# Kernel optimization log

Measured on AMD Instinct MI355X. Metric: run time of the kernel, lower is better.

Reference implementation:

```python
import jax, jax.numpy as jnp
import numpy as np

N = 100000
NEG_SLOPE = 0.2
EPS = 1e-16


def _gatconv(h_in, src, dst, W, a_src, a_dst, b):
    # h_in: [N, Fin]; src/dst: [E_tot] (self-loops included); W: [Fin, Fout]
    h = h_in @ W                                  # [N, Fout]
    alpha_s = h @ a_src                           # [N]
    alpha_d = h @ a_dst                           # [N]
    e = alpha_s[src] + alpha_d[dst]               # [E_tot]
    e = jnp.where(e > 0, e, NEG_SLOPE * e)        # leaky_relu
    m = jax.ops.segment_max(e, dst, num_segments=N)
    e = jnp.exp(e - m[dst])
    s = jax.ops.segment_sum(e, dst, num_segments=N)
    alpha = e / (s[dst] + EPS)                    # segment softmax over in-edges of each dst
    out = jax.ops.segment_sum(alpha[:, None] * h[src], dst, num_segments=N)
    return out + b


def setup_inputs() -> dict:
    key = jax.random.key(0)
    ks = jax.random.split(key, 10)
    Fin, Fh, Fo = 64, 64, 40
    E = 1600000
    x = jax.random.normal(ks[0], (N, Fin), dtype=jnp.float32)
    edge_index = jax.random.randint(ks[1], (2, E), 0, N, dtype=jnp.int64)
    g = 1.0 / np.sqrt(Fin)
    W1 = jax.random.uniform(ks[2], (Fin, Fh), jnp.float32, -g, g)
    a_src1 = jax.random.uniform(ks[3], (Fh,), jnp.float32, -g, g)
    a_dst1 = jax.random.uniform(ks[4], (Fh,), jnp.float32, -g, g)
    b1 = jnp.zeros((Fh,), jnp.float32)
    g2 = 1.0 / np.sqrt(Fh)
    W2 = jax.random.uniform(ks[5], (Fh, Fo), jnp.float32, -g2, g2)
    a_src2 = jax.random.uniform(ks[6], (Fo,), jnp.float32, -g2, g2)
    a_dst2 = jax.random.uniform(ks[7], (Fo,), jnp.float32, -g2, g2)
    b2 = jnp.zeros((Fo,), jnp.float32)
    return {"x": x, "edge_index": edge_index, "W1": W1, "a_src1": a_src1,
            "a_dst1": a_dst1, "b1": b1, "W2": W2, "a_src2": a_src2,
            "a_dst2": a_dst2, "b2": b2}


def reference(x, edge_index, W1, a_src1, a_dst1, b1, W2, a_src2, a_dst2, b2):
    # add self loops (PyG GATConv default)
    loops = jnp.arange(N, dtype=edge_index.dtype)
    src = jnp.concatenate([edge_index[0], loops])
    dst = jnp.concatenate([edge_index[1], loops])
    h = _gatconv(x, src, dst, W1, a_src1, a_dst1, b1)
    h = jax.nn.relu(h)  # dropout p=0 / eval -> no-op
    h = _gatconv(h, src, dst, W2, a_src2, a_dst2, b2)
    return jax.nn.log_softmax(h, axis=-1)
```

## Files before the change

### kernel.cpp

```cpp
#include <hip/hip_runtime.h>
#include <math.h>

#ifndef NEG_SLOPE
#define NEG_SLOPE 0.2f
#endif

#define BUCK_BITS 9
#define BUCK_SIZE 512
#define BUCK_CAP  12288
#define PA_ILP    8

__device__ __forceinline__ void get_edge(const void* ei, int is64, int e, int E,
                                         int& s, int& d) {
    if (e >= E) { s = e - E; d = s; return; }
    if (is64) {
        const long long* p = (const long long*)ei;
        s = (int)p[e];
        d = (int)p[(long long)E + e];
    } else {
        const int* p = (const int*)ei;
        s = p[e];
        d = p[E + e];
    }
}

__device__ __forceinline__ unsigned f2bf1(float x) {
    unsigned u = __float_as_uint(x);
    return (u + 0x7fffu + ((u >> 16) & 1u)) >> 16;
}

__global__ __launch_bounds__(256) void bin_gemm1(
    const void* __restrict__ ei, int E, int Etot, int binB,
    int* __restrict__ fill, int2* __restrict__ pairs,
    const float* __restrict__ x, const float* __restrict__ W1,
    const float* __restrict__ avs, const float* __restrict__ avd,
    unsigned short* __restrict__ Hb, float* __restrict__ asn,
    float* __restrict__ adn, int N) {
    __shared__ __align__(16) char smem[34816];
    const int t = threadIdx.x;

    if ((int)blockIdx.x < binB) {
        int* cnt   = (int*)smem;
        int* goff  = cnt + 256;
        int* sflag = goff + 256;
        if (t < 64) {
            const int* p = (const int*)ei;
            int bad = 0;
            for (int j = 0; j < 4; ++j) bad |= (p[2 * (t * 4 + j) + 1] != 0);
            unsigned long long m = __ballot(bad);
            if (t == 0) *sflag = (m == 0ull) ? 1 : 0;
        }
        cnt[t] = 0;
        __syncthreads();
        const int is64 = *sflag;
        const int base = blockIdx.x * (256 * PA_ILP) + t;
        int s[PA_ILP], d[PA_ILP], r[PA_ILP];
        bool ok[PA_ILP];
#pragma unroll
        for (int u = 0; u < PA_ILP; ++u) {
            int e = base + u * 256;
            ok[u] = (e < Etot);
            s[u] = d[u] = 0;
            if (ok[u]) get_edge(ei, is64, e, E, s[u], d[u]);
        }
#pragma unroll
        for (int u = 0; u < PA_ILP; ++u)
            if (ok[u]) r[u] = atomicAdd(&cnt[d[u] >> BUCK_BITS], 1);
        __syncthreads();
        if (cnt[t] > 0) goff[t] = atomicAdd(&fill[t], cnt[t]);
        __syncthreads();
#pragma unroll
        for (int u = 0; u < PA_ILP; ++u) {
            if (ok[u]) {
                int b = d[u] >> BUCK_BITS;
                int idx = goff[b] + r[u];
                if (idx < BUCK_CAP)
                    pairs[(size_t)b * BUCK_CAP + idx] = make_int2(s[u], d[u]);
            }
        }
    } else {
        constexpr int K = 64, F = 64, TPR = 4, R = 64, C = 16;
        float* sW  = (float*)smem;
        float* sA  = sW + K * F;
        float* sas = sA + R * (K + 4);
        float* sad = sas + F;

        for (int i = t; i < K * F / 4; i += 256)
            ((float4*)sW)[i] = ((const float4*)W1)[i];
        for (int i = t; i < F; i += 256) { sas[i] = avs[i]; sad[i] = avd[i]; }

        const int base = (blockIdx.x - binB) * R;
        for (int i = t; i < R * (K / 4); i += 256) {
            int row = i >> 4;
            int c4  = i & 15;
            float4 v = make_float4(0.f, 0.f, 0.f, 0.f);
            if (base + row < N)
                v = ((const float4*)(x + (size_t)(base + row) * K))[c4];
            float* dp = &sA[row * (K + 4) + c4 * 4];
            dp[0] = v.x; dp[1] = v.y; dp[2] = v.z; dp[3] = v.w;
        }
        __syncthreads();

        const int r  = t / TPR;
        const int f0 = (t % TPR) * C;
        float acc[C];
#pragma unroll
        for (int j = 0; j < C; ++j) acc[j] = 0.f;
        const float* sa = &sA[r * (K + 4)];
#pragma unroll
        for (int k = 0; k < K; ++k) {
            float av = sa[k];
            const float* w = &sW[k * F + f0];
#pragma unroll
            for (int j = 0; j < C; ++j) acc[j] += av * w[j];
        }
        float ps = 0.f, pd = 0.f;
#pragma unroll
        for (int j = 0; j < C; ++j) { ps += acc[j] * sas[f0 + j]; pd += acc[j] * sad[f0 + j]; }
#pragma unroll
        for (int off = 1; off < TPR; off <<= 1) {
            ps += __shfl_xor(ps, off);
            pd += __shfl_xor(pd, off);
        }
        const int row = base + r;
        if (row < N) {
            if ((t % TPR) == 0) { asn[row] = ps; adn[row] = pd; }
            unsigned* hp = (unsigned*)(Hb + (size_t)row * F + f0);
#pragma unroll
            for (int j = 0; j < C / 2; ++j)
                hp[j] = f2bf1(acc[2 * j]) | (f2bf1(acc[2 * j + 1]) << 16);
        }
    }
}

__global__ __launch_bounds__(256) void bucket_csr(
    const int2* __restrict__ pairs, const int* __restrict__ fill,
    int* __restrict__ row_ptr, int* __restrict__ csr_src, int N, int nbuck) {
    __shared__ int cnt[BUCK_SIZE];
    __shared__ int offs[BUCK_SIZE];
    __shared__ int sbase[256];
    __shared__ int stot;
    const int t = threadIdx.x;
    if (t < 64) {
        int v[4];
        int loc = 0;
#pragma unroll
        for (int i = 0; i < 4; ++i) {
            int idx = t * 4 + i;
            v[i] = (idx < nbuck) ? fill[idx] : 0;
            loc += v[i];
        }
        int x = loc;
        for (int off = 1; off < 64; off <<= 1) {
            int y = __shfl_up(x, off);
            if (t >= off) x += y;
        }
        int run = x - loc;
#pragma unroll
        for (int i = 0; i < 4; ++i) {
            int idx = t * 4 + i;
            if (idx < 256) sbase[idx] = run;
            run += v[i];
        }
        if (t == 63) stot = x;
    }
    cnt[t] = 0; cnt[t + 256] = 0;
    __syncthreads();

    const int b = blockIdx.x;
    const int base_d = b << BUCK_BITS;
    const int gb = sbase[b];
    int m = fill[b];
    if (m > BUCK_CAP) m = BUCK_CAP;
    if (b == 0 && t == 0) row_ptr[N] = stot;
    const int2* bp = pairs + (size_t)b * BUCK_CAP;

    int i = t;
    for (; i + 768 < m; i += 1024) {
        int2 p0 = bp[i], p1 = bp[i + 256], p2 = bp[i + 512], p3 = bp[i + 768];
        atomicAdd(&cnt[p0.y - base_d], 1);
        atomicAdd(&cnt[p1.y - base_d], 1);
        atomicAdd(&cnt[p2.y - base_d], 1);
        atomicAdd(&cnt[p3.y - base_d], 1);
    }
    for (; i < m; i += 256) atomicAdd(&cnt[bp[i].y - base_d], 1);
    __syncthreads();

    if (t < 64) {
        int v[8];
        int loc = 0;
#pragma unroll
        for (int j = 0; j < 8; ++j) { v[j] = cnt[t * 8 + j]; loc += v[j]; }
        int x = loc;
        for (int off = 1; off < 64; off <<= 1) {
            int y = __shfl_up(x, off);
            if (t >= off) x += y;
        }
        int run = x - loc;
#pragma unroll
        for (int j = 0; j < 8; ++j) { offs[t * 8 + j] = gb + run; run += v[j]; }
    }
    __syncthreads();

    for (int k = t; k < BUCK_SIZE; k += 256) {
        int d = base_d + k;
        if (d < N) row_ptr[d] = offs[k];
    }
    __syncthreads();

    i = t;
    for (; i + 768 < m; i += 1024) {
        int2 p0 = bp[i], p1 = bp[i + 256], p2 = bp[i + 512], p3 = bp[i + 768];
        csr_src[atomicAdd(&offs[p0.y - base_d], 1)] = p0.x;
        csr_src[atomicAdd(&offs[p1.y - base_d], 1)] = p1.x;
        csr_src[atomicAdd(&offs[p2.y - base_d], 1)] = p2.x;
        csr_src[atomicAdd(&offs[p3.y - base_d], 1)] = p3.x;
    }
    for (; i < m; i += 256) {
        int2 p = bp[i];
        csr_src[atomicAdd(&offs[p.y - base_d], 1)] = p.x;
    }
}

__device__ __forceinline__ void bf16x8_fma(uint4 hv, float w, float* acc) {
    const unsigned* u = (const unsigned*)&hv;
#pragma unroll
    for (int i = 0; i < 4; ++i) {
        float lo = __uint_as_float(u[i] << 16);
        float hi = __uint_as_float(u[i] & 0xffff0000u);
        acc[2 * i]     += w * lo;
        acc[2 * i + 1] += w * hi;
    }
}

__global__ __launch_bounds__(256) void agg1_gemm2(
    const int* __restrict__ row_ptr, const int* __restrict__ csr_src,
    const float* __restrict__ asn1, const float* __restrict__ adn1,
    const unsigned short* __restrict__ Hb, const float* __restrict__ b1,
    const float* __restrict__ W2, const float* __restrict__ a_s2,
    const float* __restrict__ a_d2, unsigned short* __restrict__ Hb2,
    float* __restrict__ asn2, float* __restrict__ adn2, int N) {
    __shared__ float sW2[64 * 40];
    __shared__ float sa2[40], sd2[40], sb1[64];
    __shared__ float rowbuf[16][68];
    const int t = threadIdx.x;
    for (int i = t; i < 640; i += 256) ((float4*)sW2)[i] = ((const float4*)W2)[i];
    if (t < 40) { sa2[t] = a_s2[t]; sd2[t] = a_d2[t]; }
    if (t >= 64 && t < 128) sb1[t - 64] = b1[t - 64];
    __syncthreads();

    const int lane    = t & 63;
    const int sub     = lane & 15;
    const int half    = sub >> 3;
    const int q       = sub & 7;
    const int grpbase = lane & 48;
    const int slot    = t >> 4;
    const int node    = blockIdx.x * 16 + slot;
    const bool valid  = node < N;
    const int nd      = valid ? node : N - 1;

    const int r0 = row_ptr[nd], r1 = row_ptr[nd + 1];
    const float add = adn1[nd];

    float acc[8];
#pragma unroll
    for (int i = 0; i < 8; ++i) acc[i] = 0.f;
    float Ssum = 0.f;

    for (int base = r0; base < r1; base += 16) {
        int cnt = r1 - base;
        if (cnt > 16) cnt = 16;
        int s = 0;
        float w = 0.f;
        if (sub < cnt) {
            s = csr_src[base + sub];
            float v = asn1[s] + add;
            v = v > 0.f ? v : NEG_SLOPE * v;
            w = __expf(v);
        }
        Ssum += w;
        for (int j = 0; j < cnt; j += 8) {
            int se[4]; float we[4]; uint4 hv[4];
#pragma unroll
            for (int k = 0; k < 4; ++k) {
                int e = j + 2 * k + half;
                int src_lane = grpbase | (e & 15);
                se[k] = __shfl(s, src_lane);
                float wk = __shfl(w, src_lane);
                we[k] = (e < cnt) ? wk : 0.f;
            }
#pragma unroll
            for (int k = 0; k < 4; ++k)
                hv[k] = *(const uint4*)(Hb + (size_t)se[k] * 64 + q * 8);
#pragma unroll
            for (int k = 0; k < 4; ++k) bf16x8_fma(hv[k], we[k], acc);
        }
    }
#pragma unroll
    for (int i = 0; i < 8; ++i) acc[i] += __shfl_xor(acc[i], 8);
#pragma unroll
    for (int off = 1; off < 16; off <<= 1) Ssum += __shfl_xor(Ssum, off);
    const float inv = 1.f / (Ssum + 1e-16f);

    float row[8];
#pragma unroll
    for (int i = 0; i < 8; ++i) row[i] = fmaxf(acc[i] * inv + sb1[q * 8 + i], 0.f);
    if (half == 0) {
#pragma unroll
        for (int i = 0; i < 8; ++i) rowbuf[slot][q * 8 + i] = row[i];
    }

    const bool m2 = (sub + 32) < 40;
    const int f2c = m2 ? sub + 32 : 39;
    float h2a = 0.f, h2b = 0.f, h2c = 0.f;
#pragma unroll 8
    for (int k = 0; k < 64; ++k) {
        float a = rowbuf[slot][k];
        h2a += a * sW2[k * 40 + sub];
        h2b += a * sW2[k * 40 + sub + 16];
        h2c += a * sW2[k * 40 + f2c];
    }
    float ps = h2a * sa2[sub] + h2b * sa2[sub + 16] + (m2 ? h2c * sa2[sub + 32] : 0.f);
    float pd = h2a * sd2[sub] + h2b * sd2[sub + 16] + (m2 ? h2c * sd2[sub + 32] : 0.f);
#pragma unroll
    for (int off = 1; off < 16; off <<= 1) {
        ps += __shfl_xor(ps, off);
        pd += __shfl_xor(pd, off);
    }
    if (valid) {
        unsigned short* hp = Hb2 + (size_t)node * 40;
        hp[sub]      = (unsigned short)f2bf1(h2a);
        hp[sub + 16] = (unsigned short)f2bf1(h2b);
        if (m2) hp[sub + 32] = (unsigned short)f2bf1(h2c);
        if (sub == 0) { asn2[node] = ps; adn2[node] = pd; }
    }
}

__global__ __launch_bounds__(256) void agg2_lsm(
    const int* __restrict__ row_ptr, const int* __restrict__ csr_src,
    const float* __restrict__ asn, const float* __restrict__ adn,
    const unsigned short* __restrict__ Hb, const float* __restrict__ bias,
    float* __restrict__ out, int N) {
    constexpr int F = 40, NC = 5;
    const int lane    = threadIdx.x & 63;
    const int sub     = lane & 15;
    const int half    = sub >> 3;
    const int q       = sub & 7;
    const int grpbase = lane & 48;
    const int node    = blockIdx.x * 16 + (threadIdx.x >> 4);
    const bool valid  = node < N;
    const int nd      = valid ? node : N - 1;
    const int qc      = (q < NC) ? q : NC - 1;
    const float qmask = (q < NC) ? 1.f : 0.f;

    const int r0 = row_ptr[nd], r1 = row_ptr[nd + 1];
    const float add = adn[nd];

    float acc[8];
#pragma unroll
    for (int i = 0; i < 8; ++i) acc[i] = 0.f;
    float Ssum = 0.f;

    for (int base = r0; base < r1; base += 16) {
        int cnt = r1 - base;
        if (cnt > 16) cnt = 16;
        int s = 0;
        float w = 0.f;
        if (sub < cnt) {
            s = csr_src[base + sub];
            float v = asn[s] + add;
            v = v > 0.f ? v : NEG_SLOPE * v;
            w = __expf(v);
        }
        Ssum += w;
        for (int j = 0; j < cnt; j += 8) {
            int se[4]; float we[4]; uint4 hv[4];
#pragma unroll
            for (int k = 0; k < 4; ++k) {
                int e = j + 2 * k + half;
                int src_lane = grpbase | (e & 15);
                se[k] = __shfl(s, src_lane);
                float wk = __shfl(w, src_lane) * qmask;
                we[k] = (e < cnt) ? wk : 0.f;
            }
#pragma unroll
            for (int k = 0; k < 4; ++k)
                hv[k] = *(const uint4*)(Hb + (size_t)se[k] * F + qc * 8);
#pragma unroll
            for (int k = 0; k < 4; ++k) bf16x8_fma(hv[k], we[k], acc);
        }
    }
#pragma unroll
    for (int i = 0; i < 8; ++i) acc[i] += __shfl_xor(acc[i], 8);
#pragma unroll
    for (int off = 1; off < 16; off <<= 1) Ssum += __shfl_xor(Ssum, off);
    const float inv = 1.f / (Ssum + 1e-16f);
    float r[8];
#pragma unroll
    for (int i = 0; i < 8; ++i) r[i] = acc[i] * inv;

    float val[8];
#pragma unroll
    for (int i = 0; i < 8; ++i) val[i] = r[i] + bias[qc * 8 + i];
    float mx = -3.0e38f;
    if (q < NC) {
#pragma unroll
        for (int i = 0; i < 8; ++i) mx = fmaxf(mx, val[i]);
    }
#pragma unroll
    for (int off = 1; off <= 4; off <<= 1) mx = fmaxf(mx, __shfl_xor(mx, off));
    float sm = 0.f;
    if (q < NC) {
#pragma unroll
        for (int i = 0; i < 8; ++i) sm += __expf(val[i] - mx);
    }
#pragma unroll
    for (int off = 1; off <= 4; off <<= 1) sm += __shfl_xor(sm, off);
    float ls = logf(sm) + mx;
    if (valid && half == 0 && q < NC) {
        float* op = out + (size_t)node * F + q * 8;
        ((float4*)op)[0] = make_float4(val[0] - ls, val[1] - ls, val[2] - ls, val[3] - ls);
        ((float4*)op)[1] = make_float4(val[4] - ls, val[5] - ls, val[6] - ls, val[7] - ls);
    }
}

extern "C" void kernel_launch(void* const* d_in, const int* in_sizes, int n_in,
                              void* d_out, int out_size, void* d_ws, size_t ws_size,
                              hipStream_t stream) {
    const float* x   = (const float*)d_in[0];
    const void*  ei  = d_in[1];
    const float* W1  = (const float*)d_in[2];
    const float* as1 = (const float*)d_in[3];
    const float* ad1 = (const float*)d_in[4];
    const float* b1  = (const float*)d_in[5];
    const float* W2  = (const float*)d_in[6];
    const float* as2 = (const float*)d_in[7];
    const float* ad2 = (const float*)d_in[8];
    const float* b2  = (const float*)d_in[9];
    float* out = (float*)d_out;

    const int N     = in_sizes[0] / 64;
    const int E     = in_sizes[1] / 2;
    const int Etot  = E + N;
    const int nbuck = (N + BUCK_SIZE - 1) >> BUCK_BITS;

    float* ws = (float*)d_ws;
    unsigned short* hb  = (unsigned short*)ws;  ws += (size_t)N * 32;
    unsigned short* hb2 = (unsigned short*)ws;  ws += (size_t)N * 20;
    float* asn1 = ws;              ws += N;
    float* adn1 = ws;              ws += N;
    float* asn2 = ws;              ws += N;
    float* adn2 = ws;              ws += N;
    int* row_ptr = (int*)ws;       ws += N + 1;
    int* csr_src = (int*)ws;       ws += Etot;
    int* fill   = (int*)ws;        ws += 256;
    int2* pairs = (int2*)ws;       ws += (size_t)256 * BUCK_CAP * 2;

    const int binB  = (Etot + 256 * PA_ILP - 1) / (256 * PA_ILP);
    const int gemmB = (N + 63) / 64;
    const int AGG_B = (N + 15) / 16;

    hipMemsetAsync(fill, 0, 256 * sizeof(int), stream);
    bin_gemm1<<<binB + gemmB, 256, 0, stream>>>(
        ei, E, Etot, binB, fill, pairs, x, W1, as1, ad1, hb, asn1, adn1, N);
    bucket_csr<<<nbuck, 256, 0, stream>>>(pairs, fill, row_ptr, csr_src, N, nbuck);
    agg1_gemm2<<<AGG_B, 256, 0, stream>>>(
        row_ptr, csr_src, asn1, adn1, hb, b1, W2, as2, ad2, hb2, asn2, adn2, N);
    agg2_lsm<<<AGG_B, 256, 0, stream>>>(
        row_ptr, csr_src, asn2, adn2, hb2, b2, out, N);
}
```

Measured before the change: 246.8 us.

## Pack binned edge pairs into 32-bit words and interleave bin/GEMM blocks

The edge-binning pass now stores each edge as one 32-bit word holding the 17-bit source and the 9-bit in-bucket destination, where it used to store an int2. This halves the pair buffer written by bin_gemm1 and read twice by bucket_csr. The bin and GEMM1 blocks are interleaved by a fixed period so atomic/scatter-heavy blocks run alongside compute blocks. GEMM1 now reads x rows straight from global memory as float4 instead of staging them in LDS, which shrinks shared memory per block and may raise occupancy. The packing assumes node ids fit in 17 bits.

Measured after the change: 226.9 us. -8.1%, faster.

```diff
diff --git a/kernel.cpp b/kernel.cpp
--- a/kernel.cpp
+++ b/kernel.cpp
@@ -9,6 +9,7 @@
 #define BUCK_SIZE 512
 #define BUCK_CAP  12288
 #define PA_ILP    8
+#define SMAX      0x1FFFF
 
 __device__ __forceinline__ void get_edge(const void* ei, int is64, int e, int E,
                                          int& s, int& d) {
@@ -30,16 +31,19 @@
 }
 
 __global__ __launch_bounds__(256) void bin_gemm1(
-    const void* __restrict__ ei, int E, int Etot, int binB,
-    int* __restrict__ fill, int2* __restrict__ pairs,
+    const void* __restrict__ ei, int E, int Etot, int binB, int gemmB, int period,
+    int* __restrict__ fill, unsigned* __restrict__ pairs,
     const float* __restrict__ x, const float* __restrict__ W1,
     const float* __restrict__ avs, const float* __restrict__ avd,
     unsigned short* __restrict__ Hb, float* __restrict__ asn,
     float* __restrict__ adn, int N) {
-    __shared__ __align__(16) char smem[34816];
+    __shared__ __align__(16) char smem[16896];
     const int t = threadIdx.x;
-
-    if ((int)blockIdx.x < binB) {
+    const int bi = blockIdx.x;
+    const bool isBin = (bi % period) == 0;
+
+    if (isBin) {
+        const int bb = bi / period;
         int* cnt   = (int*)smem;
         int* goff  = cnt + 256;
         int* sflag = goff + 256;
@@ -53,7 +57,7 @@
         cnt[t] = 0;
         __syncthreads();
         const int is64 = *sflag;
-        const int base = blockIdx.x * (256 * PA_ILP) + t;
+        const int base = bb * (256 * PA_ILP) + t;
         int s[PA_ILP], d[PA_ILP], r[PA_ILP];
         bool ok[PA_ILP];
 #pragma unroll
@@ -75,44 +79,43 @@
                 int b = d[u] >> BUCK_BITS;
                 int idx = goff[b] + r[u];
                 if (idx < BUCK_CAP)
-                    pairs[(size_t)b * BUCK_CAP + idx] = make_int2(s[u], d[u]);
+                    pairs[(size_t)b * BUCK_CAP + idx] =
+                        (unsigned)s[u] | ((unsigned)(d[u] & (BUCK_SIZE - 1)) << 17);
             }
         }
     } else {
+        const int gi = bi - bi / period - 1;
+        if (gi >= gemmB) return;
         constexpr int K = 64, F = 64, TPR = 4, R = 64, C = 16;
         float* sW  = (float*)smem;
-        float* sA  = sW + K * F;
-        float* sas = sA + R * (K + 4);
+        float* sas = sW + K * F;
         float* sad = sas + F;
 
         for (int i = t; i < K * F / 4; i += 256)
             ((float4*)sW)[i] = ((const float4*)W1)[i];
-        for (int i = t; i < F; i += 256) { sas[i] = avs[i]; sad[i] = avd[i]; }
-
-        const int base = (blockIdx.x - binB) * R;
-        for (int i = t; i < R * (K / 4); i += 256) {
-            int row = i >> 4;
-            int c4  = i & 15;
-            float4 v = make_float4(0.f, 0.f, 0.f, 0.f);
-            if (base + row < N)
-                v = ((const float4*)(x + (size_t)(base + row) * K))[c4];
-            float* dp = &sA[row * (K + 4) + c4 * 4];
-            dp[0] = v.x; dp[1] = v.y; dp[2] = v.z; dp[3] = v.w;
-        }
+        if (t < F) { sas[t] = avs[t]; sad[t] = avd[t]; }
         __syncthreads();
 
+        const int base = gi * R;
         const int r  = t / TPR;
         const int f0 = (t % TPR) * C;
+        const int row = base + r;
         float acc[C];
 #pragma unroll
         for (int j = 0; j < C; ++j) acc[j] = 0.f;
-        const float* sa = &sA[r * (K + 4)];
-#pragma unroll
-        for (int k = 0; k < K; ++k) {
-            float av = sa[k];
-            const float* w = &sW[k * F + f0];
-#pragma unroll
-            for (int j = 0; j < C; ++j) acc[j] += av * w[j];
+        if (row < N) {
+            const float4* xr = (const float4*)(x + (size_t)row * K);
+#pragma unroll
+            for (int c4 = 0; c4 < 16; ++c4) {
+                float4 a = xr[c4];
+                const float* w0 = &sW[(c4 * 4 + 0) * F + f0];
+                const float* w1 = &sW[(c4 * 4 + 1) * F + f0];
+                const float* w2 = &sW[(c4 * 4 + 2) * F + f0];
+                const float* w3 = &sW[(c4 * 4 + 3) * F + f0];
+#pragma unroll
+                for (int j = 0; j < C; ++j)
+                    acc[j] += a.x * w0[j] + a.y * w1[j] + a.z * w2[j] + a.w * w3[j];
+            }
         }
         float ps = 0.f, pd = 0.f;
 #pragma unroll
@@ -122,7 +125,6 @@
             ps += __shfl_xor(ps, off);
             pd += __shfl_xor(pd, off);
         }
-        const int row = base + r;
         if (row < N) {
             if ((t % TPR) == 0) { asn[row] = ps; adn[row] = pd; }
             unsigned* hp = (unsigned*)(Hb + (size_t)row * F + f0);
@@ -134,7 +136,7 @@
 }
 
 __global__ __launch_bounds__(256) void bucket_csr(
-    const int2* __restrict__ pairs, const int* __restrict__ fill,
+    const unsigned* __restrict__ pairs, const int* __restrict__ fill,
     int* __restrict__ row_ptr, int* __restrict__ csr_src, int N, int nbuck) {
     __shared__ int cnt[BUCK_SIZE];
     __shared__ int offs[BUCK_SIZE];
@@ -168,22 +170,21 @@
     __syncthreads();
 
     const int b = blockIdx.x;
-    const int base_d = b << BUCK_BITS;
     const int gb = sbase[b];
     int m = fill[b];
     if (m > BUCK_CAP) m = BUCK_CAP;
     if (b == 0 && t == 0) row_ptr[N] = stot;
-    const int2* bp = pairs + (size_t)b * BUCK_CAP;
+    const unsigned* bp = pairs + (size_t)b * BUCK_CAP;
 
     int i = t;
     for (; i + 768 < m; i += 1024) {
-        int2 p0 = bp[i], p1 = bp[i + 256], p2 = bp[i + 512], p3 = bp[i + 768];
-        atomicAdd(&cnt[p0.y - base_d], 1);
-        atomicAdd(&cnt[p1.y - base_d], 1);
-        atomicAdd(&cnt[p2.y - base_d], 1);
-        atomicAdd(&cnt[p3.y - base_d], 1);
-    }
-    for (; i < m; i += 256) atomicAdd(&cnt[bp[i].y - base_d], 1);
+        unsigned p0 = bp[i], p1 = bp[i + 256], p2 = bp[i + 512], p3 = bp[i + 768];
+        atomicAdd(&cnt[p0 >> 17], 1);
+        atomicAdd(&cnt[p1 >> 17], 1);
+        atomicAdd(&cnt[p2 >> 17], 1);
+        atomicAdd(&cnt[p3 >> 17], 1);
+    }
+    for (; i < m; i += 256) atomicAdd(&cnt[bp[i] >> 17], 1);
     __syncthreads();
 
     if (t < 64) {
@@ -202,6 +203,7 @@
     }
     __syncthreads();
 
+    const int base_d = b << BUCK_BITS;
     for (int k = t; k < BUCK_SIZE; k += 256) {
         int d = base_d + k;
         if (d < N) row_ptr[d] = offs[k];
@@ -210,15 +212,15 @@
 
     i = t;
     for (; i + 768 < m; i += 1024) {
-        int2 p0 = bp[i], p1 = bp[i + 256], p2 = bp[i + 512], p3 = bp[i + 768];
-        csr_src[atomicAdd(&offs[p0.y - base_d], 1)] = p0.x;
-        csr_src[atomicAdd(&offs[p1.y - base_d], 1)] = p1.x;
-        csr_src[atomicAdd(&offs[p2.y - base_d], 1)] = p2.x;
-        csr_src[atomicAdd(&offs[p3.y - base_d], 1)] = p3.x;
+        unsigned p0 = bp[i], p1 = bp[i + 256], p2 = bp[i + 512], p3 = bp[i + 768];
+        csr_src[atomicAdd(&offs[p0 >> 17], 1)] = p0 & SMAX;
+        csr_src[atomicAdd(&offs[p1 >> 17], 1)] = p1 & SMAX;
+        csr_src[atomicAdd(&offs[p2 >> 17], 1)] = p2 & SMAX;
+        csr_src[atomicAdd(&offs[p3 >> 17], 1)] = p3 & SMAX;
     }
     for (; i < m; i += 256) {
-        int2 p = bp[i];
-        csr_src[atomicAdd(&offs[p.y - base_d], 1)] = p.x;
+        unsigned p = bp[i];
+        csr_src[atomicAdd(&offs[p >> 17], 1)] = p & SMAX;
     }
 }
 
@@ -454,15 +456,18 @@
     int* row_ptr = (int*)ws;       ws += N + 1;
     int* csr_src = (int*)ws;       ws += Etot;
     int* fill   = (int*)ws;        ws += 256;
-    int2* pairs = (int2*)ws;       ws += (size_t)256 * BUCK_CAP * 2;
-
-    const int binB  = (Etot + 256 * PA_ILP - 1) / (256 * PA_ILP);
-    const int gemmB = (N + 63) / 64;
-    const int AGG_B = (N + 15) / 16;
+    unsigned* pairs = (unsigned*)ws;  ws += (size_t)256 * BUCK_CAP;
+
+    const int binB   = (Etot + 256 * PA_ILP - 1) / (256 * PA_ILP);
+    const int gemmB  = (N + 63) / 64;
+    const int period = gemmB / binB + 2;
+    const int grid1  = binB * period;
+    const int AGG_B  = (N + 15) / 16;
 
     hipMemsetAsync(fill, 0, 256 * sizeof(int), stream);
-    bin_gemm1<<<binB + gemmB, 256, 0, stream>>>(
-        ei, E, Etot, binB, fill, pairs, x, W1, as1, ad1, hb, asn1, adn1, N);
+    bin_gemm1<<<grid1, 256, 0, stream>>>(
+        ei, E, Etot, binB, gemmB, period, fill, pairs,
+        x, W1, as1, ad1, hb, asn1, adn1, N);
     bucket_csr<<<nbuck, 256, 0, stream>>>(pairs, fill, row_ptr, csr_src, N, nbuck);
     agg1_gemm2<<<AGG_B, 256, 0, stream>>>(
         row_ptr, csr_src, asn1, adn1, hb, b1, W2, as2, ad2, hb2, asn2, adn2, N);
```
